# Kernel optimization log

Measured on AMD Instinct MI355X. Metric: run time of the kernel, lower is better.

## Reference

```python
import jax, jax.numpy as jnp
import numpy as np
from jax.scipy.special import logsumexp

EPS = 1e-4  # self.epsilon in the original module


def _pairwise_sqdist(a, b):
    # a: [B,n,d], b: [B,m,d] -> [B,n,m]; same math as get_distance (sum_d a^2+b^2-2ab)
    return (jnp.sum(a * a, axis=-1)[:, :, None]
            + jnp.sum(b * b, axis=-1)[:, None, :]
            - 2.0 * jnp.einsum('bnd,bmd->bnm', a, b))


def setup_inputs() -> dict:
    key = jax.random.key(0)
    kx, ky, ka, kb = jax.random.split(key, 4)
    b, t, n, m, d = 4, 16, 2048, 2048, 64
    return {
        'x': jax.random.normal(kx, (b, t, n, d), dtype=jnp.float32),
        'y': jax.random.normal(ky, (b, t, m, d), dtype=jnp.float32),
        'loga': jax.random.normal(ka, (b, t, n), dtype=jnp.float32),
        'logb': jax.random.normal(kb, (b, t, m), dtype=jnp.float32),
    }


def reference(x, y, loga, logb):
    b, t, n, d = x.shape
    m = y.shape[2]
    # time-major for scan
    xt = jnp.moveaxis(x, 1, 0)      # [t,b,n,d]
    yt = jnp.moveaxis(y, 1, 0)      # [t,b,m,d]
    lat = jnp.moveaxis(loga, 1, 0)  # [t,b,n]
    lbt = jnp.moveaxis(logb, 1, 0)  # [t,b,m]

    def step(carry, inp):
        f_prev, g_prev = carry
        x_new, y_new, x_prev, y_prev, la_prev, lb_prev, la_new = inp
        D = _pairwise_sqdist(x_new, y_prev)  # [b,n,m]
        f_new = -EPS * logsumexp((-D + g_prev[:, None, :]) / EPS + lb_prev[:, None, :], axis=2)
        D2 = _pairwise_sqdist(y_new, x_prev)  # [b,m,n]
        g_new = -EPS * logsumexp((-D2 + f_prev[:, None, :]) / EPS + la_prev[:, None, :], axis=2)
        # Original forward passes loga[:, i] for BOTH new_loga and new_logb (faithful).
        # loss is a global sum (scalar) that torch broadcasts into losses[:, i].
        loss = jnp.sum(jnp.exp(la_new) * f_new) + jnp.sum(jnp.exp(la_new) * g_new)
        return (f_new, g_new), (loss, f_new, g_new)

    f0 = jnp.zeros((b, n), x.dtype)
    g0 = jnp.zeros((b, m), x.dtype)
    xs = (xt[1:], yt[1:], xt[:-1], yt[:-1], lat[:-1], lbt[:-1], lat[1:])
    _, (loss_seq, f_seq, g_seq) = jax.lax.scan(step, (f0, g0), xs)

    losses = jnp.concatenate(
        [jnp.zeros((b, 1), x.dtype), jnp.broadcast_to(loss_seq[None, :], (b, t - 1))], axis=1)
    f = jnp.concatenate([f0[:, None, :], jnp.moveaxis(f_seq, 0, 1)], axis=1)  # [b,t,n]
    g = jnp.concatenate([g0[:, None, :], jnp.moveaxis(g_seq, 0, 1)], axis=1)  # [b,t,m]
    return losses, f, g
```

## Files before the change

### kernel.cpp

```cpp
#include <hip/hip_runtime.h>

#define Bq 4
#define Tt 16
#define Nn 2048
#define Dd 64
#define EPSc 1e-4f

typedef __attribute__((ext_vector_type(4))) int intx4;

__device__ __forceinline__ int pack4i(int a, int b, int c, int d) {
    return (a & 255) | ((b & 255) << 8) | ((c & 255) << 16) | ((d & 255) << 24);
}

__device__ __forceinline__ void load_lds16(const void* gptr, void* lptr) {
    __builtin_amdgcn_global_load_lds(
        (const __attribute__((address_space(1))) unsigned int*)gptr,
        (__attribute__((address_space(3))) unsigned int*)lptr,
        16, 0, 0);
}

__device__ __forceinline__ void stage8k(const char* __restrict__ g, char* lds, int w, int l) {
    load_lds16(g + w * 1024 + l * 16, lds + w * 1024);
}

__global__ void convert_kernel(const float* __restrict__ x, const float* __restrict__ y,
                               char* __restrict__ qxh, char* __restrict__ qxl,
                               char* __restrict__ qyh, char* __restrict__ qyl,
                               float* __restrict__ sxs, float* __restrict__ sys,
                               float* __restrict__ sqx, float* __restrict__ sqy,
                               float* __restrict__ pf0, float* __restrict__ pg0,
                               float* __restrict__ out_f, float* __restrict__ out_g,
                               float* __restrict__ loss_ws)
{
    const int tid = threadIdx.x;
    const int l = tid & 63;
    const int row = blockIdx.x * 32 + (tid >> 6) * 8 + (l >> 3);
    const int q = l & 7;
    const int g = q >> 1;
    const int sw = (row >> 1) & 3;
    const size_t dstb = (size_t)row * 64 + ((g ^ sw) << 4) + (q & 1) * 8;

    const float4* px = reinterpret_cast<const float4*>(x + (size_t)row * 64 + q * 8);
    float4 u0 = px[0], u1 = px[1];
    float fx[8] = {u0.x, u0.y, u0.z, u0.w, u1.x, u1.y, u1.z, u1.w};
    float ssx = 0.f, amx = 0.f;
#pragma unroll
    for (int e = 0; e < 8; ++e) {
        ssx = fmaf(fx[e], fx[e], ssx);
        amx = fmaxf(amx, fabsf(fx[e]));
    }
#pragma unroll
    for (int d = 1; d < 8; d <<= 1) {
        ssx += __shfl_xor(ssx, d, 64);
        amx = fmaxf(amx, __shfl_xor(amx, d, 64));
    }
    amx = fmaxf(amx, 1e-8f);
    const float s1x = amx * (1.f / 127.f);
    const float i1x = 127.f / amx;
    const float i2x = i1x * 254.f;
    int ih[8], il[8];
#pragma unroll
    for (int e = 0; e < 8; ++e) {
        float hq = rintf(fx[e] * i1x);
        hq = fminf(fmaxf(hq, -127.f), 127.f);
        ih[e] = (int)hq;
        const float r = fmaf(-s1x, hq, fx[e]);
        float lq = rintf(r * i2x);
        lq = fminf(fmaxf(lq, -127.f), 127.f);
        il[e] = (int)lq;
    }
    *reinterpret_cast<int2*>(qxh + dstb) = make_int2(pack4i(ih[0], ih[1], ih[2], ih[3]),
                                                    pack4i(ih[4], ih[5], ih[6], ih[7]));
    *reinterpret_cast<int2*>(qxl + dstb) = make_int2(pack4i(il[0], il[1], il[2], il[3]),
                                                    pack4i(il[4], il[5], il[6], il[7]));

    const float4* py = reinterpret_cast<const float4*>(y + (size_t)row * 64 + q * 8);
    float4 v0 = py[0], v1 = py[1];
    float fy[8] = {v0.x, v0.y, v0.z, v0.w, v1.x, v1.y, v1.z, v1.w};
    float ssy = 0.f, amy = 0.f;
#pragma unroll
    for (int e = 0; e < 8; ++e) {
        ssy = fmaf(fy[e], fy[e], ssy);
        amy = fmaxf(amy, fabsf(fy[e]));
    }
#pragma unroll
    for (int d = 1; d < 8; d <<= 1) {
        ssy += __shfl_xor(ssy, d, 64);
        amy = fmaxf(amy, __shfl_xor(amy, d, 64));
    }
    amy = fmaxf(amy, 1e-8f);
    const float s1y = amy * (1.f / 127.f);
    const float i1y = 127.f / amy;
    const float i2y = i1y * 254.f;
#pragma unroll
    for (int e = 0; e < 8; ++e) {
        float hq = rintf(fy[e] * i1y);
        hq = fminf(fmaxf(hq, -127.f), 127.f);
        ih[e] = (int)hq;
        const float r = fmaf(-s1y, hq, fy[e]);
        float lq = rintf(r * i2y);
        lq = fminf(fmaxf(lq, -127.f), 127.f);
        il[e] = (int)lq;
    }
    *reinterpret_cast<int2*>(qyh + dstb) = make_int2(pack4i(ih[0], ih[1], ih[2], ih[3]),
                                                    pack4i(ih[4], ih[5], ih[6], ih[7]));
    *reinterpret_cast<int2*>(qyl + dstb) = make_int2(pack4i(il[0], il[1], il[2], il[3]),
                                                    pack4i(il[4], il[5], il[6], il[7]));

    if (q == 0) {
        sxs[row] = s1x;
        sys[row] = s1y;
        sqx[row] = ssx;
        sqy[row] = ssy;
        const int t = (row >> 11) & 15, b = row >> 15, n = row & (Nn - 1);
        if (t == 0) {
            out_f[(size_t)b * Tt * Nn + n] = 0.f;
            out_g[(size_t)b * Tt * Nn + n] = 0.f;
#pragma unroll
            for (int h = 0; h < 2; ++h) {
                pf0[((size_t)b * 2 + h) * Nn + n] = -ssx;
                pg0[((size_t)b * 2 + h) * Nn + n] = -ssy;
            }
        }
    }
    if (blockIdx.x == 0 && tid < Tt) loss_ws[tid] = 0.f;
}

__launch_bounds__(512, 2)
__global__ void minmat_kernel(const char* __restrict__ qxh, const char* __restrict__ qxl,
                              const char* __restrict__ qyh, const char* __restrict__ qyl,
                              const float* __restrict__ sxs, const float* __restrict__ sys,
                              const float* __restrict__ loga, const float* __restrict__ logb,
                              const float* __restrict__ sqx, const float* __restrict__ sqy,
                              const float* __restrict__ pf_in, const float* __restrict__ pg_in,
                              float* __restrict__ pf_out, float* __restrict__ pg_out,
                              float* __restrict__ out_f, float* __restrict__ out_g,
                              float* __restrict__ loss_ws, int s)
{
    __shared__ __align__(16) char Ah[8192], Al[8192];
    __shared__ __align__(16) char Bh[2][8192], Bl[2][8192];
    __shared__ __align__(16) float carr[1024];
    __shared__ __align__(16) float tarr[1024];
    __shared__ __align__(16) float sarr[128];
    __shared__ float redm[512];

    const int tid = threadIdx.x;
    const int w = tid >> 6, l = tid & 63;
    const int flat = blockIdx.x;
    const int z = flat & 7;
    const int b = z >> 1;
    const int which = (z & 1) ^ (s & 1);
    const int rr0 = flat >> 3;
    const int i0 = (rr0 & 15) * 128;
    const int jh = rr0 >> 4;
    const int jbase = jh * 1024;

    const size_t curm = ((size_t)b * Tt + s) * Nn;
    const size_t prvm = curm - Nn;

    const char* Ahs = (which ? qyh : qxh) + (curm + i0) * 64;
    const char* Als = (which ? qyl : qxl) + (curm + i0) * 64;
    const char* Bhs = (which ? qxh : qyh) + (prvm + jbase) * 64;
    const char* Bls = (which ? qxl : qyl) + (prvm + jbase) * 64;
    const float* ascale = (which ? sys : sxs) + curm + i0;
    const float* bscale = (which ? sxs : sys) + prvm + jbase;
    const float* pin  = which ? pf_in : pg_in;
    float* pout       = which ? pg_out : pf_out;
    const float* clog = (which ? loga : logb) + prvm + jbase;

    stage8k(Ahs, Ah, w, l);
    stage8k(Als, Al, w, l);
    stage8k(Bhs, Bh[0], w, l);
    stage8k(Bls, Bl[0], w, l);

#pragma unroll
    for (int e = 0; e < 2; ++e) {
        const int jj = tid * 2 + e;
        const float p0 = pin[((size_t)b * 2) * Nn + jbase + jj];
        const float p1 = pin[((size_t)b * 2 + 1) * Nn + jbase + jj];
        carr[jj] = -fminf(p0, p1) - EPSc * clog[jj];
        tarr[jj] = bscale[jj];
    }
    if (tid < 128) sarr[tid] = ascale[tid];
    __syncthreads();

    const int wr = w >> 2, wc = w & 3;
    const int m0 = wr * 64, n0 = wc * 32;
    const int r15 = l & 15, g = l >> 4;
    const int csel = ((g ^ ((r15 >> 1) & 3)) << 4);

    intx4 ahr[4], alr[4];
#pragma unroll
    for (int m = 0; m < 4; ++m) {
        const int ra = (m0 + m * 16 + r15) * 64 + csel;
        ahr[m] = *reinterpret_cast<const intx4*>(&Ah[ra]);
        alr[m] = *reinterpret_cast<const intx4*>(&Al[ra]);
    }
    float4 srow4[4];
#pragma unroll
    for (int m = 0; m < 4; ++m)
        srow4[m] = *reinterpret_cast<const float4*>(&sarr[m0 + m * 16 + g * 4]);

    float mm[4][4];
#pragma unroll
    for (int m = 0; m < 4; ++m)
#pragma unroll
        for (int r2 = 0; r2 < 4; ++r2) mm[m][r2] = 1e30f;

    const float inv254 = 1.f / 254.f;

    for (int t = 0; t < 8; ++t) {
        const int p = t & 1;
        if (t < 7) {
            stage8k(Bhs + (size_t)(t + 1) * 8192, Bh[p ^ 1], w, l);
            stage8k(Bls + (size_t)(t + 1) * 8192, Bl[p ^ 1], w, l);
            asm volatile("s_waitcnt vmcnt(2)" ::: "memory");
        } else {
            asm volatile("s_waitcnt vmcnt(0)" ::: "memory");
        }
        __builtin_amdgcn_s_barrier();
        asm volatile("" ::: "memory");

        intx4 bhr[2], blr[2];
#pragma unroll
        for (int nn = 0; nn < 2; ++nn) {
            const int rb = (n0 + nn * 16 + r15) * 64 + csel;
            bhr[nn] = *reinterpret_cast<const intx4*>(&Bh[p][rb]);
            blr[nn] = *reinterpret_cast<const intx4*>(&Bl[p][rb]);
        }

        intx4 acc1[4][2], acc2[4][2];
#pragma unroll
        for (int m = 0; m < 4; ++m)
#pragma unroll
            for (int nn = 0; nn < 2; ++nn) {
                acc1[m][nn] = intx4{0, 0, 0, 0};
                acc2[m][nn] = intx4{0, 0, 0, 0};
            }
#pragma unroll
        for (int m = 0; m < 4; ++m)
#pragma unroll
            for (int nn = 0; nn < 2; ++nn) {
                acc1[m][nn] = __builtin_amdgcn_mfma_i32_16x16x64_i8(ahr[m], bhr[nn], acc1[m][nn], 0, 0, 0);
                acc2[m][nn] = __builtin_amdgcn_mfma_i32_16x16x64_i8(ahr[m], blr[nn], acc2[m][nn], 0, 0, 0);
                acc2[m][nn] = __builtin_amdgcn_mfma_i32_16x16x64_i8(alr[m], bhr[nn], acc2[m][nn], 0, 0, 0);
            }

        const int jt = t * 128 + n0;
        const float cv0 = carr[jt + r15];
        const float cv1 = carr[jt + 16 + r15];
        const float tm0 = -2.f * tarr[jt + r15];
        const float tm1 = -2.f * tarr[jt + 16 + r15];
#pragma unroll
        for (int m = 0; m < 4; ++m) {
            const float* sr = reinterpret_cast<const float*>(&srow4[m]);
#pragma unroll
            for (int r2 = 0; r2 < 4; ++r2) {
                const float p0f = fmaf(inv254, (float)acc2[m][0][r2], (float)acc1[m][0][r2]);
                const float p1f = fmaf(inv254, (float)acc2[m][1][r2], (float)acc1[m][1][r2]);
                const float v0 = fmaf(sr[r2] * tm0, p0f, cv0);
                const float v1 = fmaf(sr[r2] * tm1, p1f, cv1);
                mm[m][r2] = fminf(mm[m][r2], fminf(v0, v1));
            }
        }
        asm volatile("" ::: "memory");
        __builtin_amdgcn_s_barrier();
        asm volatile("" ::: "memory");
    }

#pragma unroll
    for (int off = 1; off < 16; off <<= 1)
#pragma unroll
        for (int m = 0; m < 4; ++m)
#pragma unroll
            for (int r2 = 0; r2 < 4; ++r2)
                mm[m][r2] = fminf(mm[m][r2], __shfl_xor(mm[m][r2], off, 64));

    if (r15 == 0) {
#pragma unroll
        for (int m = 0; m < 4; ++m)
#pragma unroll
            for (int r2 = 0; r2 < 4; ++r2)
                redm[wc * 128 + m0 + m * 16 + g * 4 + r2] = mm[m][r2];
    }
    __syncthreads();
    if (tid < 128) {
        const float v = fminf(fminf(redm[tid], redm[128 + tid]),
                              fminf(redm[256 + tid], redm[384 + tid]));
        pout[((size_t)b * 2 + jh) * Nn + i0 + tid] = v;
    }

    if (s >= 2 && tid < 32) {
        const int fr = flat * 32 + tid;
        const int fb = fr >> 11, fi = fr & (Nn - 1);
        const size_t fidx = ((size_t)fb * Tt + (s - 1)) * Nn + fi;
        const float mf = fminf(pf_in[((size_t)fb * 2) * Nn + fi],
                               pf_in[((size_t)fb * 2 + 1) * Nn + fi]);
        const float mg = fminf(pg_in[((size_t)fb * 2) * Nn + fi],
                               pg_in[((size_t)fb * 2 + 1) * Nn + fi]);
        const float fn = sqx[fidx] + mf, gn = sqy[fidx] + mg;
        out_f[fidx] = fn;
        out_g[fidx] = gn;
        float contrib = expf(loga[fidx]) * (fn + gn);
#pragma unroll
        for (int off = 16; off > 0; off >>= 1)
            contrib += __shfl_down(contrib, off, 64);
        if (tid == 0) atomicAdd(&loss_ws[s - 1], contrib);
    }
}

__global__ void finish_kernel(int u,
                              const float* __restrict__ pf, const float* __restrict__ pg,
                              const float* __restrict__ sqx, const float* __restrict__ sqy,
                              const float* __restrict__ loga,
                              float* __restrict__ out_f, float* __restrict__ out_g,
                              float* __restrict__ loss_ws)
{
    __shared__ float red8[8];
    const int tid = threadIdx.x;
    const int r = blockIdx.x * 512 + tid;
    const int b = r >> 11, i = r & (Nn - 1);
    const size_t idx = ((size_t)b * Tt + u) * Nn + i;
    const float mf = fminf(pf[((size_t)b * 2) * Nn + i], pf[((size_t)b * 2 + 1) * Nn + i]);
    const float mg = fminf(pg[((size_t)b * 2) * Nn + i], pg[((size_t)b * 2 + 1) * Nn + i]);
    const float fn = sqx[idx] + mf, gn = sqy[idx] + mg;
    out_f[idx] = fn;
    out_g[idx] = gn;
    float contrib = expf(loga[idx]) * (fn + gn);
#pragma unroll
    for (int off = 32; off > 0; off >>= 1)
        contrib += __shfl_down(contrib, off, 64);
    if ((tid & 63) == 0) red8[tid >> 6] = contrib;
    __syncthreads();
    if (tid == 0) {
        float ssum = 0.f;
#pragma unroll
        for (int k = 0; k < 8; ++k) ssum += red8[k];
        atomicAdd(&loss_ws[u], ssum);
    }
}

__global__ void final_kernel(float* __restrict__ out_losses, const float* __restrict__ loss_ws)
{
    const int tid = threadIdx.x;
    const int t = tid & 15;
    out_losses[tid] = (t == 0) ? 0.f : loss_ws[t];
}

extern "C" void kernel_launch(void* const* d_in, const int* in_sizes, int n_in,
                              void* d_out, int out_size, void* d_ws, size_t ws_size,
                              hipStream_t stream)
{
    const float* x    = (const float*)d_in[0];
    const float* y    = (const float*)d_in[1];
    const float* loga = (const float*)d_in[2];
    const float* logb = (const float*)d_in[3];

    float* out        = (float*)d_out;
    float* out_losses = out;
    float* out_f      = out + Bq * Tt;
    float* out_g      = out_f + (size_t)Bq * Tt * Nn;

    const size_t NROW = (size_t)Bq * Tt * Nn;
    char* base = (char*)d_ws;
    char* qxh = base;
    char* qxl = qxh + NROW * 64;
    char* qyh = qxl + NROW * 64;
    char* qyl = qyh + NROW * 64;
    float* sxs = (float*)(qyl + NROW * 64);
    float* sys = sxs + NROW;
    float* sqx = sys + NROW;
    float* sqy = sqx + NROW;
    const size_t PM = (size_t)Bq * 2 * Nn;
    float* pf0 = sqy + NROW;
    float* pg0 = pf0 + PM;
    float* pf1 = pg0 + PM;
    float* pg1 = pf1 + PM;
    float* loss_ws = pg1 + PM;

    convert_kernel<<<4096, 256, 0, stream>>>(x, y, qxh, qxl, qyh, qyl,
                                             sxs, sys, sqx, sqy, pf0, pg0,
                                             out_f, out_g, loss_ws);

    for (int s = 1; s < Tt; ++s) {
        const float* pf_in = (s & 1) ? pf0 : pf1;
        const float* pg_in = (s & 1) ? pg0 : pg1;
        float* pf_out = (s & 1) ? pf1 : pf0;
        float* pg_out = (s & 1) ? pg1 : pg0;
        minmat_kernel<<<256, 512, 0, stream>>>(qxh, qxl, qyh, qyl, sxs, sys,
                                               loga, logb, sqx, sqy,
                                               pf_in, pg_in, pf_out, pg_out,
                                               out_f, out_g, loss_ws, s);
    }
    finish_kernel<<<16, 512, 0, stream>>>(15, pf1, pg1, sqx, sqy, loga,
                                          out_f, out_g, loss_ws);
    final_kernel<<<1, 64, 0, stream>>>(out_losses, loss_ws);
}
```

Baseline: 335.5 us.

## Split column range into four chunks and triple-buffer B tiles in minmat

Each block now covers 512 columns instead of 1024, so the grid doubles to 512 blocks and there are four partial-min slices per row instead of two. The B tile loop is unrolled into four explicit tiles with a three-deep LDS buffer and prefetches issued earlier, and the global loads for the column constants are hoisted ahead of the staging. The int8 partial products are combined in integer arithmetic and the -2/254 factor is folded into tarr. The aim is more parallelism on a 256-CTA launch and better load/compute overlap. The cost is more LDS per block, more partial outputs to reduce, and possible int overflow in the combined accumulator.

```diff
diff --git a/kernel.cpp b/kernel.cpp
--- a/kernel.cpp
+++ b/kernel.cpp
@@ -117,14 +117,55 @@
             out_f[(size_t)b * Tt * Nn + n] = 0.f;
             out_g[(size_t)b * Tt * Nn + n] = 0.f;
 #pragma unroll
-            for (int h = 0; h < 2; ++h) {
-                pf0[((size_t)b * 2 + h) * Nn + n] = -ssx;
-                pg0[((size_t)b * 2 + h) * Nn + n] = -ssy;
+            for (int h = 0; h < 4; ++h) {
+                pf0[((size_t)b * 4 + h) * Nn + n] = -ssx;
+                pg0[((size_t)b * 4 + h) * Nn + n] = -ssy;
             }
         }
     }
     if (blockIdx.x == 0 && tid < Tt) loss_ws[tid] = 0.f;
 }
+
+#define COMPUTE_TILE(T, P)                                                      \
+    {                                                                           \
+        intx4 bhr[2], blr[2];                                                   \
+        const int rb0 = (n0 + r15) * 64 + csel;                                 \
+        const int rb1 = (n0 + 16 + r15) * 64 + csel;                            \
+        bhr[0] = *reinterpret_cast<const intx4*>(&Bh[P][rb0]);                  \
+        blr[0] = *reinterpret_cast<const intx4*>(&Bl[P][rb0]);                  \
+        bhr[1] = *reinterpret_cast<const intx4*>(&Bh[P][rb1]);                  \
+        blr[1] = *reinterpret_cast<const intx4*>(&Bl[P][rb1]);                  \
+        intx4 acc1[4][2], acc2[4][2];                                           \
+        _Pragma("unroll") for (int m = 0; m < 4; ++m)                           \
+            _Pragma("unroll") for (int nn = 0; nn < 2; ++nn) {                  \
+                acc1[m][nn] = intx4{0, 0, 0, 0};                                \
+                acc2[m][nn] = intx4{0, 0, 0, 0};                                \
+            }                                                                   \
+        _Pragma("unroll") for (int m = 0; m < 4; ++m)                           \
+            _Pragma("unroll") for (int nn = 0; nn < 2; ++nn) {                  \
+                acc1[m][nn] = __builtin_amdgcn_mfma_i32_16x16x64_i8(            \
+                    ahr[m], bhr[nn], acc1[m][nn], 0, 0, 0);                     \
+                acc2[m][nn] = __builtin_amdgcn_mfma_i32_16x16x64_i8(            \
+                    ahr[m], blr[nn], acc2[m][nn], 0, 0, 0);                     \
+                acc2[m][nn] = __builtin_amdgcn_mfma_i32_16x16x64_i8(            \
+                    alr[m], bhr[nn], acc2[m][nn], 0, 0, 0);                     \
+            }                                                                   \
+        const int jt = (T) * 128 + n0;                                          \
+        const float cv0 = carr[jt + r15];                                       \
+        const float cv1 = carr[jt + 16 + r15];                                  \
+        const float tm0 = tarr[jt + r15];                                       \
+        const float tm1 = tarr[jt + 16 + r15];                                  \
+        _Pragma("unroll") for (int m = 0; m < 4; ++m) {                         \
+            const float* sr = reinterpret_cast<const float*>(&srow4[m]);        \
+            _Pragma("unroll") for (int r2 = 0; r2 < 4; ++r2) {                  \
+                const int c0 = acc1[m][0][r2] * 254 + acc2[m][0][r2];           \
+                const int c1 = acc1[m][1][r2] * 254 + acc2[m][1][r2];           \
+                const float v0 = fmaf(sr[r2] * tm0, (float)c0, cv0);            \
+                const float v1 = fmaf(sr[r2] * tm1, (float)c1, cv1);            \
+                mm[m][r2] = fminf(mm[m][r2], fminf(v0, v1));                    \
+            }                                                                   \
+        }                                                                       \
+    }
 
 __launch_bounds__(512, 2)
 __global__ void minmat_kernel(const char* __restrict__ qxh, const char* __restrict__ qxl,
@@ -138,9 +179,9 @@
                               float* __restrict__ loss_ws, int s)
 {
     __shared__ __align__(16) char Ah[8192], Al[8192];
-    __shared__ __align__(16) char Bh[2][8192], Bl[2][8192];
-    __shared__ __align__(16) float carr[1024];
-    __shared__ __align__(16) float tarr[1024];
+    __shared__ __align__(16) char Bh[3][8192], Bl[3][8192];
+    __shared__ __align__(16) float carr[512];
+    __shared__ __align__(16) float tarr[512];
     __shared__ __align__(16) float sarr[128];
     __shared__ float redm[512];
 
@@ -152,8 +193,8 @@
     const int which = (z & 1) ^ (s & 1);
     const int rr0 = flat >> 3;
     const int i0 = (rr0 & 15) * 128;
-    const int jh = rr0 >> 4;
-    const int jbase = jh * 1024;
+    const int jq = rr0 >> 4;
+    const int jbase = jq * 512;
 
     const size_t curm = ((size_t)b * Tt + s) * Nn;
     const size_t prvm = curm - Nn;
@@ -168,105 +209,76 @@
     float* pout       = which ? pg_out : pf_out;
     const float* clog = (which ? loga : logb) + prvm + jbase;
 
+    const int jj = tid;
+    const float p0 = pin[((size_t)b * 4 + 0) * Nn + jbase + jj];
+    const float p1 = pin[((size_t)b * 4 + 1) * Nn + jbase + jj];
+    const float p2 = pin[((size_t)b * 4 + 2) * Nn + jbase + jj];
+    const float p3 = pin[((size_t)b * 4 + 3) * Nn + jbase + jj];
+    const float lg = clog[jj];
+    const float bs = bscale[jj];
+    float as_ = 0.f;
+    if (tid < 128) as_ = ascale[tid];
+
     stage8k(Ahs, Ah, w, l);
     stage8k(Als, Al, w, l);
     stage8k(Bhs, Bh[0], w, l);
     stage8k(Bls, Bl[0], w, l);
-
-#pragma unroll
-    for (int e = 0; e < 2; ++e) {
-        const int jj = tid * 2 + e;
-        const float p0 = pin[((size_t)b * 2) * Nn + jbase + jj];
-        const float p1 = pin[((size_t)b * 2 + 1) * Nn + jbase + jj];
-        carr[jj] = -fminf(p0, p1) - EPSc * clog[jj];
-        tarr[jj] = bscale[jj];
-    }
-    if (tid < 128) sarr[tid] = ascale[tid];
-    __syncthreads();
+    stage8k(Bhs + 8192, Bh[1], w, l);
+    stage8k(Bls + 8192, Bl[1], w, l);
+
+    carr[jj] = -fminf(fminf(p0, p1), fminf(p2, p3)) - EPSc * lg;
+    tarr[jj] = bs * (-2.f / 254.f);
+    if (tid < 128) sarr[tid] = as_;
+    asm volatile("s_waitcnt lgkmcnt(0)" ::: "memory");
+    __builtin_amdgcn_s_barrier();
 
     const int wr = w >> 2, wc = w & 3;
     const int m0 = wr * 64, n0 = wc * 32;
     const int r15 = l & 15, g = l >> 4;
     const int csel = ((g ^ ((r15 >> 1) & 3)) << 4);
 
+    float mm[4][4];
+#pragma unroll
+    for (int m = 0; m < 4; ++m)
+#pragma unroll
+        for (int r2 = 0; r2 < 4; ++r2) mm[m][r2] = 1e30f;
+
     intx4 ahr[4], alr[4];
+    float4 srow4[4];
+
+    stage8k(Bhs + (size_t)2 * 8192, Bh[2], w, l);
+    stage8k(Bls + (size_t)2 * 8192, Bl[2], w, l);
+    asm volatile("s_waitcnt vmcnt(4)" ::: "memory");
+    __builtin_amdgcn_s_barrier();
+
 #pragma unroll
     for (int m = 0; m < 4; ++m) {
         const int ra = (m0 + m * 16 + r15) * 64 + csel;
         ahr[m] = *reinterpret_cast<const intx4*>(&Ah[ra]);
         alr[m] = *reinterpret_cast<const intx4*>(&Al[ra]);
     }
-    float4 srow4[4];
 #pragma unroll
     for (int m = 0; m < 4; ++m)
         srow4[m] = *reinterpret_cast<const float4*>(&sarr[m0 + m * 16 + g * 4]);
 
-    float mm[4][4];
-#pragma unroll
-    for (int m = 0; m < 4; ++m)
-#pragma unroll
-        for (int r2 = 0; r2 < 4; ++r2) mm[m][r2] = 1e30f;
-
-    const float inv254 = 1.f / 254.f;
-
-    for (int t = 0; t < 8; ++t) {
-        const int p = t & 1;
-        if (t < 7) {
-            stage8k(Bhs + (size_t)(t + 1) * 8192, Bh[p ^ 1], w, l);
-            stage8k(Bls + (size_t)(t + 1) * 8192, Bl[p ^ 1], w, l);
-            asm volatile("s_waitcnt vmcnt(2)" ::: "memory");
-        } else {
-            asm volatile("s_waitcnt vmcnt(0)" ::: "memory");
-        }
-        __builtin_amdgcn_s_barrier();
-        asm volatile("" ::: "memory");
-
-        intx4 bhr[2], blr[2];
-#pragma unroll
-        for (int nn = 0; nn < 2; ++nn) {
-            const int rb = (n0 + nn * 16 + r15) * 64 + csel;
-            bhr[nn] = *reinterpret_cast<const intx4*>(&Bh[p][rb]);
-            blr[nn] = *reinterpret_cast<const intx4*>(&Bl[p][rb]);
-        }
-
-        intx4 acc1[4][2], acc2[4][2];
-#pragma unroll
-        for (int m = 0; m < 4; ++m)
-#pragma unroll
-            for (int nn = 0; nn < 2; ++nn) {
-                acc1[m][nn] = intx4{0, 0, 0, 0};
-                acc2[m][nn] = intx4{0, 0, 0, 0};
-            }
-#pragma unroll
-        for (int m = 0; m < 4; ++m)
-#pragma unroll
-            for (int nn = 0; nn < 2; ++nn) {
-                acc1[m][nn] = __builtin_amdgcn_mfma_i32_16x16x64_i8(ahr[m], bhr[nn], acc1[m][nn], 0, 0, 0);
-                acc2[m][nn] = __builtin_amdgcn_mfma_i32_16x16x64_i8(ahr[m], blr[nn], acc2[m][nn], 0, 0, 0);
-                acc2[m][nn] = __builtin_amdgcn_mfma_i32_16x16x64_i8(alr[m], bhr[nn], acc2[m][nn], 0, 0, 0);
-            }
-
-        const int jt = t * 128 + n0;
-        const float cv0 = carr[jt + r15];
-        const float cv1 = carr[jt + 16 + r15];
-        const float tm0 = -2.f * tarr[jt + r15];
-        const float tm1 = -2.f * tarr[jt + 16 + r15];
-#pragma unroll
-        for (int m = 0; m < 4; ++m) {
-            const float* sr = reinterpret_cast<const float*>(&srow4[m]);
-#pragma unroll
-            for (int r2 = 0; r2 < 4; ++r2) {
-                const float p0f = fmaf(inv254, (float)acc2[m][0][r2], (float)acc1[m][0][r2]);
-                const float p1f = fmaf(inv254, (float)acc2[m][1][r2], (float)acc1[m][1][r2]);
-                const float v0 = fmaf(sr[r2] * tm0, p0f, cv0);
-                const float v1 = fmaf(sr[r2] * tm1, p1f, cv1);
-                mm[m][r2] = fminf(mm[m][r2], fminf(v0, v1));
-            }
-        }
-        asm volatile("" ::: "memory");
-        __builtin_amdgcn_s_barrier();
-        asm volatile("" ::: "memory");
-    }
+    COMPUTE_TILE(0, 0)
+    __builtin_amdgcn_s_barrier();
+
+    stage8k(Bhs + (size_t)3 * 8192, Bh[0], w, l);
+    stage8k(Bls + (size_t)3 * 8192, Bl[0], w, l);
+    asm volatile("s_waitcnt vmcnt(4)" ::: "memory");
+    __builtin_amdgcn_s_barrier();
+    COMPUTE_TILE(1, 1)
+    __builtin_amdgcn_s_barrier();
+
+    asm volatile("s_waitcnt vmcnt(2)" ::: "memory");
+    __builtin_amdgcn_s_barrier();
+    COMPUTE_TILE(2, 2)
+    __builtin_amdgcn_s_barrier();
+
+    asm volatile("s_waitcnt vmcnt(0)" ::: "memory");
+    __builtin_amdgcn_s_barrier();
+    COMPUTE_TILE(3, 0)
 
 #pragma unroll
     for (int off = 1; off < 16; off <<= 1)
@@ -276,6 +288,7 @@
             for (int r2 = 0; r2 < 4; ++r2)
                 mm[m][r2] = fminf(mm[m][r2], __shfl_xor(mm[m][r2], off, 64));
 
+    __syncthreads();
     if (r15 == 0) {
 #pragma unroll
         for (int m = 0; m < 4; ++m)
@@ -287,23 +300,26 @@
     if (tid < 128) {
         const float v = fminf(fminf(redm[tid], redm[128 + tid]),
                               fminf(redm[256 + tid], redm[384 + tid]));
-        pout[((size_t)b * 2 + jh) * Nn + i0 + tid] = v;
-    }
-
-    if (s >= 2 && tid < 32) {
-        const int fr = flat * 32 + tid;
+        pout[((size_t)b * 4 + jq) * Nn + i0 + tid] = v;
+    }
+
+    if (s >= 2 && tid < 16) {
+        const int fr = flat * 16 + tid;
         const int fb = fr >> 11, fi = fr & (Nn - 1);
         const size_t fidx = ((size_t)fb * Tt + (s - 1)) * Nn + fi;
-        const float mf = fminf(pf_in[((size_t)fb * 2) * Nn + fi],
-                               pf_in[((size_t)fb * 2 + 1) * Nn + fi]);
-        const float mg = fminf(pg_in[((size_t)fb * 2) * Nn + fi],
-                               pg_in[((size_t)fb * 2 + 1) * Nn + fi]);
+        float mf = pf_in[((size_t)fb * 4 + 0) * Nn + fi];
+        float mg = pg_in[((size_t)fb * 4 + 0) * Nn + fi];
+#pragma unroll
+        for (int h = 1; h < 4; ++h) {
+            mf = fminf(mf, pf_in[((size_t)fb * 4 + h) * Nn + fi]);
+            mg = fminf(mg, pg_in[((size_t)fb * 4 + h) * Nn + fi]);
+        }
         const float fn = sqx[fidx] + mf, gn = sqy[fidx] + mg;
         out_f[fidx] = fn;
         out_g[fidx] = gn;
         float contrib = expf(loga[fidx]) * (fn + gn);
 #pragma unroll
-        for (int off = 16; off > 0; off >>= 1)
+        for (int off = 8; off > 0; off >>= 1)
             contrib += __shfl_down(contrib, off, 64);
         if (tid == 0) atomicAdd(&loss_ws[s - 1], contrib);
     }
@@ -321,8 +337,13 @@
     const int r = blockIdx.x * 512 + tid;
     const int b = r >> 11, i = r & (Nn - 1);
     const size_t idx = ((size_t)b * Tt + u) * Nn + i;
-    const float mf = fminf(pf[((size_t)b * 2) * Nn + i], pf[((size_t)b * 2 + 1) * Nn + i]);
-    const float mg = fminf(pg[((size_t)b * 2) * Nn + i], pg[((size_t)b * 2 + 1) * Nn + i]);
+    float mf = pf[((size_t)b * 4 + 0) * Nn + i];
+    float mg = pg[((size_t)b * 4 + 0) * Nn + i];
+#pragma unroll
+    for (int h = 1; h < 4; ++h) {
+        mf = fminf(mf, pf[((size_t)b * 4 + h) * Nn + i]);
+        mg = fminf(mg, pg[((size_t)b * 4 + h) * Nn + i]);
+    }
     const float fn = sqx[idx] + mf, gn = sqy[idx] + mg;
     out_f[idx] = fn;
     out_g[idx] = gn;
@@ -371,7 +392,7 @@
     float* sys = sxs + NROW;
     float* sqx = sys + NROW;
     float* sqy = sqx + NROW;
-    const size_t PM = (size_t)Bq * 2 * Nn;
+    const size_t PM = (size_t)Bq * 4 * Nn;
     float* pf0 = sqy + NROW;
     float* pg0 = pf0 + PM;
     float* pf1 = pg0 + PM;
@@ -387,7 +408,7 @@
         const float* pg_in = (s & 1) ? pg0 : pg1;
         float* pf_out = (s & 1) ? pf1 : pf0;
         float* pg_out = (s & 1) ? pg1 : pg0;
-        minmat_kernel<<<256, 512, 0, stream>>>(qxh, qxl, qyh, qyl, sxs, sys,
+        minmat_kernel<<<512, 512, 0, stream>>>(qxh, qxl, qyh, qyl, sxs, sys,
                                                loga, logb, sqx, sqy,
                                                pf_in, pg_in, pf_out, pg_out,
                                                out_f, out_g, loss_ws, s);
```

New measurement: 385.0 us. 14.7% more time.
